# Optimization experiments

Measured on AMD Instinct MI355X. Metric: run time of the kernel, lower is better.

The kernel has to match this reference:

```python
import jax, jax.numpy as jnp
import numpy as np

KE = 332.0636  # Coulomb constant in kcal/mol * Angstrom / e^2
N = 4096       # total sites across all frames
F = 64         # number of frames (batch_size)
M = 1024       # number of molecules


def setup_inputs() -> dict:
    key = jax.random.key(0)
    k1, k2, k3, k4, k5 = jax.random.split(key, 5)
    pos = jax.random.normal(k1, (N, 3), dtype=jnp.float32) * 10.0      # Angstrom-scale coords
    charges = jax.random.normal(k2, (N, 1), dtype=jnp.float32) * 0.5    # partial charges
    # lj_params[:, 0] = sigma, lj_params[:, 1] = epsilon (positive)
    lj_params = jax.random.uniform(k3, (N, 2), dtype=jnp.float32, minval=0.1, maxval=1.0)
    frames = jnp.sort(jax.random.randint(k4, (N,), 0, F))               # frame id per site (sorted, as in batching)
    mols = jax.random.randint(k5, (N,), 0, M)                           # molecule id per site
    return {"pos": pos, "charges": charges, "lj_params": lj_params,
            "frames": frames, "mols": mols, "num_frames": F}


def reference(pos, charges, lj_params, frames, mols, num_frames):
    # Dense ordered-pair mask: same frame, different molecule (mirrors torch.nonzero pair set)
    mask = (frames[:, None] == frames[None, :]) & (mols[:, None] != mols[None, :])  # [N, N]
    diff = pos[:, None, :] - pos[None, :, :]                                        # [N, N, 3]
    r2 = jnp.sum(diff * diff, axis=-1)                                              # [N, N]
    r = jnp.sqrt(jnp.where(mask, r2, 1.0))  # masked entries -> safe 1.0 (no div-by-zero / NaN grad)
    # Coulomb: ke * q_i * q_j / r_ij
    q = charges[:, 0]
    coul = KE * (q[:, None] * q[None, :]) / r
    # Lennard-Jones with Lorentz-Berthelot combining: sigma_ij = (s_i+s_j)/2, eps_ij = sqrt(e_i*e_j)
    sig = 0.5 * (lj_params[:, None, 0] + lj_params[None, :, 0])
    eps = jnp.sqrt(lj_params[:, None, 1] * lj_params[None, :, 1])
    sr6 = (sig / r) ** 6
    lj = 4.0 * eps * (sr6 * sr6 - sr6)
    contrib = jnp.where(mask, coul + lj, 0.0)
    # scatter(contribs, frames): pair (i,j) contributes to frame[i]; reduce rows then segment-sum
    per_site = jnp.sum(contrib, axis=1)                                             # [N]
    return jax.ops.segment_sum(per_site, frames, num_segments=num_frames)           # [num_frames]
```

## Files before the change

### kernel.cpp

```cpp
#include <hip/hip_runtime.h>

#define KE_CONST 332.0636f
constexpr int TILE = 512;

__device__ __forceinline__ int lower_bound_i(const int* __restrict__ a, int n, int key) {
    int lo = 0, len = n;
    while (len > 0) {
        int half = len >> 1;
        int mid = lo + half;
        if (a[mid] < key) { lo = mid + 1; len -= half + 1; }
        else { len = half; }
    }
    return lo;
}

__global__ __launch_bounds__(256) void lj_coul_frame_kernel(
    const float* __restrict__ pos, const float* __restrict__ charges,
    const float* __restrict__ lj, const int* __restrict__ frames,
    const int* __restrict__ mols, float* __restrict__ out, int N)
{
    const int f = blockIdx.x;
    const int tid = threadIdx.x;

    __shared__ float jx[TILE], jy[TILE], jz[TILE], jq[TILE], jsig[TILE], jse[TILE];
    __shared__ int   jmol[TILE];
    __shared__ float wsum[4];

    const int lo = lower_bound_i(frames, N, f);
    const int hi = lower_bound_i(frames, N, f + 1);

    float acc = 0.0f;

    for (int jt = lo; jt < hi; jt += TILE) {
        const int cnt = min(TILE, hi - jt);
        for (int t = tid; t < cnt; t += 256) {
            const int j = jt + t;
            jx[t]   = pos[3 * j + 0];
            jy[t]   = pos[3 * j + 1];
            jz[t]   = pos[3 * j + 2];
            jq[t]   = charges[j];
            jsig[t] = lj[2 * j + 0];
            jse[t]  = sqrtf(lj[2 * j + 1]);
            jmol[t] = mols[j];
        }
        __syncthreads();

        for (int i = lo + tid; i < hi; i += 256) {
            const float xi  = pos[3 * i + 0];
            const float yi  = pos[3 * i + 1];
            const float zi  = pos[3 * i + 2];
            const float ci  = KE_CONST * charges[i];
            const float si  = lj[2 * i + 0];
            const float sei = sqrtf(lj[2 * i + 1]);
            const int   mi  = mols[i];

            for (int t = 0; t < cnt; ++t) {
                const float dx = xi - jx[t];
                const float dy = yi - jy[t];
                const float dz = zi - jz[t];
                const float r2 = dx * dx + dy * dy + dz * dz;
                const float inv_r  = rsqrtf(r2);
                const float inv_r2 = inv_r * inv_r;
                const float coul = ci * jq[t] * inv_r;
                const float s    = si + jsig[t];
                const float sr2  = 0.25f * s * s * inv_r2;
                const float sr6  = sr2 * sr2 * sr2;
                const float ljv  = 4.0f * (sei * jse[t]) * (sr6 * sr6 - sr6);
                acc += (mi != jmol[t]) ? (coul + ljv) : 0.0f;
            }
        }
        __syncthreads();
    }

    for (int off = 32; off > 0; off >>= 1)
        acc += __shfl_down(acc, off, 64);
    if ((tid & 63) == 0) wsum[tid >> 6] = acc;
    __syncthreads();
    if (tid == 0) out[f] = wsum[0] + wsum[1] + wsum[2] + wsum[3];
}

extern "C" void kernel_launch(void* const* d_in, const int* in_sizes, int n_in,
                              void* d_out, int out_size, void* d_ws, size_t ws_size,
                              hipStream_t stream) {
    const float* pos     = (const float*)d_in[0];
    const float* charges = (const float*)d_in[1];
    const float* lj      = (const float*)d_in[2];
    const int*   frames  = (const int*)d_in[3];
    const int*   mols    = (const int*)d_in[4];
    const int    N       = in_sizes[3];
    const int    F       = out_size;

    lj_coul_frame_kernel<<<F, 256, 0, stream>>>(pos, charges, lj, frames, mols,
                                                (float*)d_out, N);
}
```

Measured before the change: 77.37 us.

## Split frame work across waves by j-stride and count frame bounds cooperatively

Replaces each thread's serial binary search for the frame bounds with a block-wide vectorized count of frames below/at f, reduced through shuffles and shared memory. The i-loop now maps 64 sites per wave, with each of the 4 waves taking every 4th j, so all waves stay busy even when a frame has fewer than 256 sites. TILE drops to 256. The count reads the whole frames array in every block, about 16 KB per block, in exchange for removing the dependent serial loads of the binary search.

```diff
diff --git a/kernel.cpp b/kernel.cpp
--- a/kernel.cpp
+++ b/kernel.cpp
@@ -1,18 +1,7 @@
 #include <hip/hip_runtime.h>
 
 #define KE_CONST 332.0636f
-constexpr int TILE = 512;
-
-__device__ __forceinline__ int lower_bound_i(const int* __restrict__ a, int n, int key) {
-    int lo = 0, len = n;
-    while (len > 0) {
-        int half = len >> 1;
-        int mid = lo + half;
-        if (a[mid] < key) { lo = mid + 1; len -= half + 1; }
-        else { len = half; }
-    }
-    return lo;
-}
+constexpr int TILE = 256;
 
 __global__ __launch_bounds__(256) void lj_coul_frame_kernel(
     const float* __restrict__ pos, const float* __restrict__ charges,
@@ -21,13 +10,37 @@
 {
     const int f = blockIdx.x;
     const int tid = threadIdx.x;
+    const int lane = tid & 63;
+    const int wv = tid >> 6;
 
     __shared__ float jx[TILE], jy[TILE], jz[TILE], jq[TILE], jsig[TILE], jse[TILE];
     __shared__ int   jmol[TILE];
+    __shared__ int   slo[4], shi[4];
     __shared__ float wsum[4];
 
-    const int lo = lower_bound_i(frames, N, f);
-    const int hi = lower_bound_i(frames, N, f + 1);
+    int c_lo = 0, c_hi = 0;
+    {
+        const int N4 = N >> 2;
+        const int4* f4 = (const int4*)frames;
+        for (int k = tid; k < N4; k += 256) {
+            const int4 v = f4[k];
+            c_lo += (v.x <  f) + (v.y <  f) + (v.z <  f) + (v.w <  f);
+            c_hi += (v.x <= f) + (v.y <= f) + (v.z <= f) + (v.w <= f);
+        }
+        for (int k = (N4 << 2) + tid; k < N; k += 256) {
+            const int v = frames[k];
+            c_lo += (v < f);
+            c_hi += (v <= f);
+        }
+        for (int off = 32; off > 0; off >>= 1) {
+            c_lo += __shfl_down(c_lo, off, 64);
+            c_hi += __shfl_down(c_hi, off, 64);
+        }
+        if (lane == 0) { slo[wv] = c_lo; shi[wv] = c_hi; }
+        __syncthreads();
+    }
+    const int lo = slo[0] + slo[1] + slo[2] + slo[3];
+    const int hi = shi[0] + shi[1] + shi[2] + shi[3];
 
     float acc = 0.0f;
 
@@ -45,7 +58,7 @@
         }
         __syncthreads();
 
-        for (int i = lo + tid; i < hi; i += 256) {
+        for (int i = lo + lane; i < hi; i += 64) {
             const float xi  = pos[3 * i + 0];
             const float yi  = pos[3 * i + 1];
             const float zi  = pos[3 * i + 2];
@@ -54,7 +67,7 @@
             const float sei = sqrtf(lj[2 * i + 1]);
             const int   mi  = mols[i];
 
-            for (int t = 0; t < cnt; ++t) {
+            for (int t = wv; t < cnt; t += 4) {
                 const float dx = xi - jx[t];
                 const float dy = yi - jy[t];
                 const float dz = zi - jz[t];
@@ -74,7 +87,7 @@
 
     for (int off = 32; off > 0; off >>= 1)
         acc += __shfl_down(acc, off, 64);
-    if ((tid & 63) == 0) wsum[tid >> 6] = acc;
+    if (lane == 0) wsum[wv] = acc;
     __syncthreads();
     if (tid == 0) out[f] = wsum[0] + wsum[1] + wsum[2] + wsum[3];
 }
```

Result: faster. 71.46 us (-7.6%).
